# Performance work log

Hardware: AMD Instinct MI355X
Metric: run time of the kernel (lower is better)

Reference implementation:

```python
import jax, jax.numpy as jnp
import numpy as np

N_NODES = 100000
N_EDGES = 1600000
IN, HID, OUT = 512, 128, 64


def setup_inputs() -> dict:
    key = jax.random.key(0)
    ks = jax.random.split(key, 7)
    x = jax.random.normal(ks[0], (N_NODES, IN), dtype=jnp.float32)
    rows = jax.random.randint(ks[1], (N_EDGES,), 0, N_NODES, dtype=jnp.int32)
    cols = jax.random.randint(ks[2], (N_EDGES,), 0, N_NODES, dtype=jnp.int32)
    vals = jax.random.uniform(ks[3], (N_EDGES,), dtype=jnp.float32)
    # torch.nn.Linear weights have shape (out_features, in_features)
    W0 = jax.random.normal(ks[4], (HID, IN), dtype=jnp.float32) * (IN ** -0.5)
    W1 = jax.random.normal(ks[5], (HID, HID), dtype=jnp.float32) * (HID ** -0.5)
    W2 = jax.random.normal(ks[6], (OUT, HID), dtype=jnp.float32) * (HID ** -0.5)
    return {"x": x, "rows": rows, "cols": cols, "vals": vals,
            "W0": W0, "W1": W1, "W2": W2}


def reference(x, rows, cols, vals, W0, W1, W2):
    n = x.shape[0]

    def spmm(h):  # out[r] = sum_e vals[e] * h[cols[e]] for rows[e] == r
        return jax.ops.segment_sum(vals[:, None] * h[cols], rows, num_segments=n)

    # layer 0: Linear -> SpMM -> ReLU (dropout p=0.0 is identity)
    h = jax.nn.relu(spmm(x @ W0.T))
    # layer 1
    h = jax.nn.relu(spmm(h @ W1.T))
    # output layer: Linear -> SpMM (no activation)
    return spmm(h @ W2.T)
```

## Files before the change

kernel.cpp:

```cpp
#include <hip/hip_runtime.h>
#include <hip/hip_bf16.h>
#include <cstddef>


typedef unsigned short ushort_t;
using frag_t = __attribute__((ext_vector_type(8))) short;
using accf4 = __attribute__((ext_vector_type(4))) float;

__device__ __forceinline__ ushort_t f2bf(float f) {
    unsigned int u = __float_as_uint(f);
    u += 0x7FFF + ((u >> 16) & 1);
    return (ushort_t)(u >> 16);
}
__device__ __forceinline__ float bf2f(unsigned int u16) {
    return __uint_as_float(u16 << 16);
}


__global__ __launch_bounds__(256) void init_k(int* __restrict__ cnt8, int m8,
                                              const float* __restrict__ W0,
                                              const float* __restrict__ W1,
                                              const float* __restrict__ W2,
                                              ushort_t* __restrict__ Wb0,
                                              ushort_t* __restrict__ Wb1,
                                              ushort_t* __restrict__ Wb2) {
    int i = blockIdx.x * 256 + threadIdx.x;
    if (i < m8) cnt8[i] = 0;
    if (i < 65536) Wb0[i] = f2bf(W0[i]);
    else if (i < 81920) Wb1[i - 65536] = f2bf(W1[i - 65536]);
    else if (i < 90112) Wb2[i - 81920] = f2bf(W2[i - 81920]);
}


__global__ __launch_bounds__(256) void block_totals(const int* __restrict__ counts,
                                                    int* __restrict__ bsums, int n) {
    __shared__ int s[256];
    int t = threadIdx.x;
    int i = blockIdx.x * 256 + t;
    s[t] = (i < n) ? counts[i] : 0;
    __syncthreads();
    for (int off = 128; off > 0; off >>= 1) {
        if (t < off) s[t] += s[t + off];
        __syncthreads();
    }
    if (t == 0) bsums[blockIdx.x] = s[0];
}

__global__ __launch_bounds__(512) void scan_sums(int* bsums, int nb) {
    __shared__ int s[512];
    int t = threadIdx.x;
    int v = (t < nb) ? bsums[t] : 0;
    s[t] = v;
    __syncthreads();
    for (int off = 1; off < 512; off *= 2) {
        int u = (t >= off) ? s[t - off] : 0;
        __syncthreads();
        s[t] += u;
        __syncthreads();
    }
    if (t < nb) bsums[t] = s[t] - v;
}

__global__ __launch_bounds__(256) void scan_wo(const int* __restrict__ data,
                                               const int* __restrict__ offs,
                                               int* __restrict__ out0, int m) {
    __shared__ int s[256];
    int t = threadIdx.x;
    int i = blockIdx.x * 256 + t;
    int v = (i < m) ? data[i] : 0;
    s[t] = v;
    __syncthreads();
    for (int off = 1; off < 256; off *= 2) {
        int u = (t >= off) ? s[t - off] : 0;
        __syncthreads();
        s[t] += u;
        __syncthreads();
    }
    if (i < m) out0[i] = s[t] - v + offs[blockIdx.x];
}

__global__ __launch_bounds__(256) void scan_final(const int* __restrict__ cnt8,
                                                  const int* __restrict__ offs,
                                                  int* __restrict__ dstbase,
                                                  int* __restrict__ row_ptr,
                                                  int n, int ne, int m8) {
    __shared__ int s[256];
    int t = threadIdx.x;
    int i = blockIdx.x * 256 + t;
    int v = (i < m8) ? cnt8[(i & 7) * n + (i >> 3)] : 0;
    s[t] = v;
    __syncthreads();
    for (int off = 1; off < 256; off *= 2) {
        int u = (t >= off) ? s[t - off] : 0;
        __syncthreads();
        s[t] += u;
        __syncthreads();
    }
    int excl = s[t] - v + offs[blockIdx.x];
    if (i < m8) {
        dstbase[i] = excl;
        if ((i & 7) == 0) row_ptr[i >> 3] = excl;
    }
    if (i == 0) row_ptr[n] = ne;
}


__global__ __launch_bounds__(256) void hist8_k(const int* __restrict__ rows,
                                               int* __restrict__ cnt8,
                                               int* __restrict__ rank,
                                               int n, int ne) {
    int e = blockIdx.x * 256 + threadIdx.x;
    if (e >= ne) return;
    int s = blockIdx.x & 7;
    rank[e] = atomicAdd(&cnt8[s * n + rows[e]], 1);
}

__global__ __launch_bounds__(256) void scatter8_k(const int* __restrict__ rows,
                                                  const int* __restrict__ cols,
                                                  const float* __restrict__ vals,
                                                  const int* __restrict__ dstbase,
                                                  const int* __restrict__ rank,
                                                  int2* __restrict__ es, int ne) {
    int e = blockIdx.x * 256 + threadIdx.x;
    if (e >= ne) return;
    int s = blockIdx.x & 7;
    int r = rows[e];
    int p = dstbase[r * 8 + s] + rank[e];
    es[p] = make_int2(cols[e], __float_as_int(vals[e]));
}


template <int K, int N, int BM, int BN, int BK, bool ABF16>
__global__ __launch_bounds__(256) void gemm_bf16(const void* __restrict__ Av,
                                                 const ushort_t* __restrict__ Wb,
                                                 ushort_t* __restrict__ C, int M) {
    constexpr int WM = BM / 2, WN = BN / 2;
    constexpr int TI = WM / 16, TJ = WN / 16;
    constexpr int LDA = BK + 8;
    constexpr int T = K / BK;
    constexpr int A_PER_F = BM * BK / 4 / 256;
    constexpr int A_PER_B = BM * BK / 8 / 256;
    constexpr int B_PER = BN * BK / 8 / 256;

    __shared__ __align__(16) ushort_t As[BM][LDA];
    __shared__ __align__(16) ushort_t Bs[BN][LDA];

    const int tid = threadIdx.x;
    const int lane = tid & 63;
    const int wid = tid >> 6;
    const int wm = wid >> 1, wn = wid & 1;
    const int rowBase = blockIdx.x * BM;
    const int lrow = lane & 15, kq = lane >> 4;

    float4 aF[ABF16 ? 1 : A_PER_F];
    uint4 aB[ABF16 ? A_PER_B : 1];
    uint4 bR[B_PER];

    auto loadTile = [&](int k0) {
        if constexpr (ABF16) {
            const ushort_t* A = (const ushort_t*)Av;
#pragma unroll
            for (int i = 0; i < A_PER_B; i++) {
                int idx = tid + i * 256;
                int r = idx / (BK / 8), c8 = idx % (BK / 8);
                int grow = rowBase + r;
                aB[i] = (grow < M) ? *(const uint4*)(A + (size_t)grow * K + k0 + c8 * 8)
                                   : make_uint4(0, 0, 0, 0);
            }
        } else {
            const float* A = (const float*)Av;
#pragma unroll
            for (int i = 0; i < A_PER_F; i++) {
                int idx = tid + i * 256;
                int r = idx / (BK / 4), c4 = idx % (BK / 4);
                int grow = rowBase + r;
                aF[i] = (grow < M) ? *(const float4*)(A + (size_t)grow * K + k0 + c4 * 4)
                                   : make_float4(0.f, 0.f, 0.f, 0.f);
            }
        }
#pragma unroll
        for (int i = 0; i < B_PER; i++) {
            int idx = tid + i * 256;
            int r = idx / (BK / 8), c8 = idx % (BK / 8);
            bR[i] = *(const uint4*)(Wb + (size_t)r * K + k0 + c8 * 8);
        }
    };
    auto storeTile = [&]() {
        if constexpr (ABF16) {
#pragma unroll
            for (int i = 0; i < A_PER_B; i++) {
                int idx = tid + i * 256;
                int r = idx / (BK / 8), c8 = idx % (BK / 8);
                *(uint4*)&As[r][c8 * 8] = aB[i];
            }
        } else {
#pragma unroll
            for (int i = 0; i < A_PER_F; i++) {
                int idx = tid + i * 256;
                int r = idx / (BK / 4), c4 = idx % (BK / 4);
                ushort_t p[4] = {f2bf(aF[i].x), f2bf(aF[i].y), f2bf(aF[i].z), f2bf(aF[i].w)};
                *(uint2*)&As[r][c4 * 4] = *(uint2*)p;
            }
        }
#pragma unroll
        for (int i = 0; i < B_PER; i++) {
            int idx = tid + i * 256;
            int r = idx / (BK / 8), c8 = idx % (BK / 8);
            *(uint4*)&Bs[r][c8 * 8] = bR[i];
        }
    };

    accf4 acc[TI][TJ];
#pragma unroll
    for (int i = 0; i < TI; i++)
#pragma unroll
        for (int j = 0; j < TJ; j++) acc[i][j] = accf4{0.f, 0.f, 0.f, 0.f};

    loadTile(0);
    storeTile();
    __syncthreads();

    for (int t = 0; t < T; t++) {
        if (t + 1 < T) loadTile((t + 1) * BK);
#pragma unroll
        for (int ks = 0; ks < BK / 32; ks++) {
            const int kb = ks * 32 + kq * 8;
            frag_t a[TI], b[TJ];
#pragma unroll
            for (int i = 0; i < TI; i++)
                a[i] = *(const frag_t*)&As[wm * WM + i * 16 + lrow][kb];
#pragma unroll
            for (int j = 0; j < TJ; j++)
                b[j] = *(const frag_t*)&Bs[wn * WN + j * 16 + lrow][kb];
#pragma unroll
            for (int i = 0; i < TI; i++)
#pragma unroll
                for (int j = 0; j < TJ; j++)
                    acc[i][j] = __builtin_amdgcn_mfma_f32_16x16x32_bf16(
                        a[i], b[j], acc[i][j], 0, 0, 0);
        }
        __syncthreads();
        if (t + 1 < T) {
            storeTile();
            __syncthreads();
        }
    }

#pragma unroll
    for (int i = 0; i < TI; i++) {
#pragma unroll
        for (int j = 0; j < TJ; j++) {
            int col = wn * WN + j * 16 + lrow;
#pragma unroll
            for (int r = 0; r < 4; r++) {
                int grow = rowBase + wm * WM + i * 16 + kq * 4 + r;
                if (grow < M) C[(size_t)grow * N + col] = f2bf(acc[i][j][r]);
            }
        }
    }
}


__device__ __forceinline__ void acc8(float* acc, uint4 q, float v) {
    acc[0] += v * bf2f(q.x & 0xffff); acc[1] += v * bf2f(q.x >> 16);
    acc[2] += v * bf2f(q.y & 0xffff); acc[3] += v * bf2f(q.y >> 16);
    acc[4] += v * bf2f(q.z & 0xffff); acc[5] += v * bf2f(q.z >> 16);
    acc[6] += v * bf2f(q.w & 0xffff); acc[7] += v * bf2f(q.w >> 16);
}
__device__ __forceinline__ void acc4f(float* acc, uint2 q, float v) {
    acc[0] += v * bf2f(q.x & 0xffff); acc[1] += v * bf2f(q.x >> 16);
    acc[2] += v * bf2f(q.y & 0xffff); acc[3] += v * bf2f(q.y >> 16);
}

template <bool RELU>
__global__ __launch_bounds__(256) void spmm_csr_128(const int* __restrict__ row_ptr,
                                                    const int2* __restrict__ es,
                                                    const ushort_t* __restrict__ G,
                                                    ushort_t* __restrict__ H, int n) {
    int row = blockIdx.x * 4 + (threadIdx.x >> 6);
    int lane = threadIdx.x & 63;
    int g = lane >> 4, lg = lane & 15;
    if (row >= n) return;
    int s = row_ptr[row];
    int e = row_ptr[row + 1];
    float acc[8];
#pragma unroll
    for (int k = 0; k < 8; k++) acc[k] = 0.f;
    const ushort_t* __restrict__ Gp = G + lg * 8;
    int p = s;
    for (; p + 15 < e; p += 16) {
        int2 e0 = es[p + g], e1 = es[p + 4 + g];
        int2 e2 = es[p + 8 + g], e3 = es[p + 12 + g];
        uint4 q0 = *(const uint4*)(Gp + (size_t)e0.x * 128);
        uint4 q1 = *(const uint4*)(Gp + (size_t)e1.x * 128);
        uint4 q2 = *(const uint4*)(Gp + (size_t)e2.x * 128);
        uint4 q3 = *(const uint4*)(Gp + (size_t)e3.x * 128);
        acc8(acc, q0, __int_as_float(e0.y));
        acc8(acc, q1, __int_as_float(e1.y));
        acc8(acc, q2, __int_as_float(e2.y));
        acc8(acc, q3, __int_as_float(e3.y));
    }
    for (; p < e; p += 4) {
        if (p + g < e) {
            int2 e0 = es[p + g];
            uint4 q0 = *(const uint4*)(Gp + (size_t)e0.x * 128);
            acc8(acc, q0, __int_as_float(e0.y));
        }
    }
#pragma unroll
    for (int k = 0; k < 8; k++) {
        acc[k] += __shfl_xor(acc[k], 16);
        acc[k] += __shfl_xor(acc[k], 32);
    }
    if (g == 0) {
        if (RELU) {
#pragma unroll
            for (int k = 0; k < 8; k++) acc[k] = fmaxf(acc[k], 0.f);
        }
        uint4 o;
        o.x = (unsigned)f2bf(acc[0]) | ((unsigned)f2bf(acc[1]) << 16);
        o.y = (unsigned)f2bf(acc[2]) | ((unsigned)f2bf(acc[3]) << 16);
        o.z = (unsigned)f2bf(acc[4]) | ((unsigned)f2bf(acc[5]) << 16);
        o.w = (unsigned)f2bf(acc[6]) | ((unsigned)f2bf(acc[7]) << 16);
        *(uint4*)(H + (size_t)row * 128 + lg * 8) = o;
    }
}

__global__ __launch_bounds__(256) void spmm_csr_64f(const int* __restrict__ row_ptr,
                                                    const int2* __restrict__ es,
                                                    const ushort_t* __restrict__ G,
                                                    float* __restrict__ H, int n) {
    int row = blockIdx.x * 4 + (threadIdx.x >> 6);
    int lane = threadIdx.x & 63;
    int g = lane >> 4, lg = lane & 15;
    if (row >= n) return;
    int s = row_ptr[row];
    int e = row_ptr[row + 1];
    float acc[4] = {0.f, 0.f, 0.f, 0.f};
    const ushort_t* __restrict__ Gp = G + lg * 4;
    int p = s;
    for (; p + 15 < e; p += 16) {
        int2 e0 = es[p + g], e1 = es[p + 4 + g];
        int2 e2 = es[p + 8 + g], e3 = es[p + 12 + g];
        uint2 q0 = *(const uint2*)(Gp + (size_t)e0.x * 64);
        uint2 q1 = *(const uint2*)(Gp + (size_t)e1.x * 64);
        uint2 q2 = *(const uint2*)(Gp + (size_t)e2.x * 64);
        uint2 q3 = *(const uint2*)(Gp + (size_t)e3.x * 64);
        acc4f(acc, q0, __int_as_float(e0.y));
        acc4f(acc, q1, __int_as_float(e1.y));
        acc4f(acc, q2, __int_as_float(e2.y));
        acc4f(acc, q3, __int_as_float(e3.y));
    }
    for (; p < e; p += 4) {
        if (p + g < e) {
            int2 e0 = es[p + g];
            uint2 q0 = *(const uint2*)(Gp + (size_t)e0.x * 64);
            acc4f(acc, q0, __int_as_float(e0.y));
        }
    }
#pragma unroll
    for (int k = 0; k < 4; k++) {
        acc[k] += __shfl_xor(acc[k], 16);
        acc[k] += __shfl_xor(acc[k], 32);
    }
    if (g == 0) {
        float4 o = make_float4(acc[0], acc[1], acc[2], acc[3]);
        *(float4*)(H + (size_t)row * 64 + lg * 4) = o;
    }
}

static inline size_t align_up(size_t x, size_t a) { return (x + a - 1) & ~(a - 1); }

extern "C" void kernel_launch(void* const* d_in, const int* in_sizes, int n_in,
                              void* d_out, int out_size, void* d_ws, size_t ws_size,
                              hipStream_t stream) {
    const float* x = (const float*)d_in[0];
    const int* rows = (const int*)d_in[1];
    const int* cols = (const int*)d_in[2];
    const float* vals = (const float*)d_in[3];
    const float* W0 = (const float*)d_in[4];
    const float* W1 = (const float*)d_in[5];
    const float* W2 = (const float*)d_in[6];
    float* out = (float*)d_out;

    const int IN = 512, HID = 128, OUT = 64;
    const int n = in_sizes[0] / IN;
    const int ne = in_sizes[1];
    (void)OUT;

    char* ws = (char*)d_ws;
    size_t off = 0;
    ushort_t* g = (ushort_t*)(ws + off); off = align_up(off + (size_t)n * HID * 2, 512);
    ushort_t* h = (ushort_t*)(ws + off); off = align_up(off + (size_t)n * HID * 2, 512);
    int2* es2 = (int2*)(ws + off); off = align_up(off + (size_t)ne * 8, 512);
    int* cnt8 = (int*)(ws + off); off = align_up(off + (size_t)8 * n * 4, 512);
    int* rank = (int*)(ws + off); off = align_up(off + (size_t)ne * 4, 512);
    int* dstbase = (int*)(ws + off); off = align_up(off + (size_t)8 * n * 4, 512);
    int* row_ptr = (int*)(ws + off); off = align_up(off + (size_t)(n + 1) * 4, 512);
    int* bsum0 = (int*)(ws + off); off = align_up(off + 4096 * 4, 512);
    int* bsum1 = (int*)(ws + off); off = align_up(off + 512 * 4, 512);
    int* off0 = (int*)(ws + off); off = align_up(off + 4096 * 4, 512);
    ushort_t* Wb0 = (ushort_t*)(ws + off); off = align_up(off + (size_t)HID * IN * 2, 512);
    ushort_t* Wb1 = (ushort_t*)(ws + off); off = align_up(off + (size_t)HID * HID * 2, 512);
    ushort_t* Wb2 = (ushort_t*)(ws + off); off = align_up(off + (size_t)OUT * HID * 2, 512);

    const int eb = (ne + 255) / 256;
    const int m8 = 8 * n;
    const int nb8 = (m8 + 255) / 256;
    const int nb8b = (nb8 + 255) / 256;

    init_k<<<nb8, 256, 0, stream>>>(cnt8, m8, W0, W1, W2, Wb0, Wb1, Wb2);
    hist8_k<<<eb, 256, 0, stream>>>(rows, cnt8, rank, n, ne);
    block_totals<<<nb8, 256, 0, stream>>>(cnt8, bsum0, m8);
    (void)0;
    {
        struct Launcher {};
    }
    extern __global__ void block_totals_t(const int*, int*, int, int);
    block_totals_t<<<nb8, 256, 0, stream>>>(cnt8, bsum0, n, m8);
    block_totals<<<nb8b, 256, 0, stream>>>(bsum0, bsum1, nb8);
    scan_sums<<<1, 512, 0, stream>>>(bsum1, nb8b);
    scan_wo<<<nb8b, 256, 0, stream>>>(bsum0, bsum1, off0, nb8);
    scan_final<<<nb8, 256, 0, stream>>>(cnt8, off0, dstbase, row_ptr, n, ne, m8);
    scatter8_k<<<eb, 256, 0, stream>>>(rows, cols, vals, dstbase, rank, es2, ne);

    const int gblocks = (n + 127) / 128;
    const int sblocks = (n + 3) / 4;

    gemm_bf16<512, 128, 128, 128, 64, false><<<gblocks, 256, 0, stream>>>(x, Wb0, g, n);
    spmm_csr_128<true><<<sblocks, 256, 0, stream>>>(row_ptr, es2, g, h, n);

    gemm_bf16<128, 128, 128, 128, 64, true><<<gblocks, 256, 0, stream>>>(h, Wb1, g, n);
    spmm_csr_128<true><<<sblocks, 256, 0, stream>>>(row_ptr, es2, g, h, n);

    gemm_bf16<128, 64, 128, 64, 64, true><<<gblocks, 256, 0, stream>>>(h, Wb2, g, n);
    spmm_csr_64f<<<sblocks, 256, 0, stream>>>(row_ptr, es2, g, out, n);
}

__global__ __launch_bounds__(256) void block_totals_t(const int* __restrict__ cnt8,
                                                      int* __restrict__ bsums,
                                                      int n, int m8) {
    __shared__ int s[256];
    int t = threadIdx.x;
    int i = blockIdx.x * 256 + t;
    s[t] = (i < m8) ? cnt8[(i & 7) * n + (i >> 3)] : 0;
    __syncthreads();
    for (int off = 128; off > 0; off >>= 1) {
        if (t < off) s[t] += s[t + off];
        __syncthreads();
    }
    if (t == 0) bsums[blockIdx.x] = s[0];
}
```

Before: 661.6 us.

## Fuse layer GEMMs into SpMM epilogues and merge first GEMM with init

Moves the layer-1 and layer-2 dense GEMMs into the epilogue of the preceding SpMM: each block aggregates 16 rows, applies ReLU, stages them in shared memory, and multiplies by the bf16 weights with MFMA before writing. The first GEMM now reads fp32 W0 directly and runs in the same launch as the counter reset and weight conversion. This removes two GEMM launches and their intermediate round trips through global memory, at the cost of fewer threads per row during the gather and extra shared-memory and sync overhead in the SpMM kernels. It also drops a redundant block_totals launch.

Result: no change. 666.7 us (+0.8%).

```diff
diff --git a/kernel.cpp b/kernel.cpp
--- a/kernel.cpp
+++ b/kernel.cpp
@@ -17,18 +17,129 @@
 }
 
 
-__global__ __launch_bounds__(256) void init_k(int* __restrict__ cnt8, int m8,
-                                              const float* __restrict__ W0,
-                                              const float* __restrict__ W1,
-                                              const float* __restrict__ W2,
-                                              ushort_t* __restrict__ Wb0,
-                                              ushort_t* __restrict__ Wb1,
-                                              ushort_t* __restrict__ Wb2) {
-    int i = blockIdx.x * 256 + threadIdx.x;
-    if (i < m8) cnt8[i] = 0;
-    if (i < 65536) Wb0[i] = f2bf(W0[i]);
-    else if (i < 81920) Wb1[i - 65536] = f2bf(W1[i - 65536]);
-    else if (i < 90112) Wb2[i - 81920] = f2bf(W2[i - 81920]);
+__device__ void gemm0_body(int bx, const float* __restrict__ A,
+                           const float* __restrict__ W, ushort_t* __restrict__ C,
+                           int M) {
+    constexpr int K = 512, N = 128, BM = 128, BN = 128, BK = 64;
+    constexpr int WM = BM / 2, WN = BN / 2;
+    constexpr int TI = WM / 16, TJ = WN / 16;
+    constexpr int LDA = BK + 8;
+    constexpr int T = K / BK;
+    constexpr int A_PER = BM * BK / 4 / 256;
+    constexpr int B_PER = BN * BK / 4 / 256;
+
+    __shared__ __align__(16) ushort_t As[BM][LDA];
+    __shared__ __align__(16) ushort_t Bs[BN][LDA];
+
+    const int tid = threadIdx.x;
+    const int lane = tid & 63;
+    const int wid = tid >> 6;
+    const int wm = wid >> 1, wn = wid & 1;
+    const int rowBase = bx * BM;
+    const int lrow = lane & 15, kq = lane >> 4;
+
+    float4 aF[A_PER], bF[B_PER];
+
+    auto loadTile = [&](int k0) {
+#pragma unroll
+        for (int i = 0; i < A_PER; i++) {
+            int idx = tid + i * 256;
+            int r = idx / (BK / 4), c4 = idx % (BK / 4);
+            int grow = rowBase + r;
+            aF[i] = (grow < M) ? *(const float4*)(A + (size_t)grow * K + k0 + c4 * 4)
+                               : make_float4(0.f, 0.f, 0.f, 0.f);
+        }
+#pragma unroll
+        for (int i = 0; i < B_PER; i++) {
+            int idx = tid + i * 256;
+            int r = idx / (BK / 4), c4 = idx % (BK / 4);
+            bF[i] = *(const float4*)(W + (size_t)r * K + k0 + c4 * 4);
+        }
+    };
+    auto storeTile = [&]() {
+#pragma unroll
+        for (int i = 0; i < A_PER; i++) {
+            int idx = tid + i * 256;
+            int r = idx / (BK / 4), c4 = idx % (BK / 4);
+            ushort_t p[4] = {f2bf(aF[i].x), f2bf(aF[i].y), f2bf(aF[i].z), f2bf(aF[i].w)};
+            *(uint2*)&As[r][c4 * 4] = *(uint2*)p;
+        }
+#pragma unroll
+        for (int i = 0; i < B_PER; i++) {
+            int idx = tid + i * 256;
+            int r = idx / (BK / 4), c4 = idx % (BK / 4);
+            ushort_t p[4] = {f2bf(bF[i].x), f2bf(bF[i].y), f2bf(bF[i].z), f2bf(bF[i].w)};
+            *(uint2*)&Bs[r][c4 * 4] = *(uint2*)p;
+        }
+    };
+
+    accf4 acc[TI][TJ];
+#pragma unroll
+    for (int i = 0; i < TI; i++)
+#pragma unroll
+        for (int j = 0; j < TJ; j++) acc[i][j] = accf4{0.f, 0.f, 0.f, 0.f};
+
+    loadTile(0);
+    storeTile();
+    __syncthreads();
+
+    for (int t = 0; t < T; t++) {
+        if (t + 1 < T) loadTile((t + 1) * BK);
+#pragma unroll
+        for (int ks = 0; ks < BK / 32; ks++) {
+            const int kb = ks * 32 + kq * 8;
+            frag_t a[TI], b[TJ];
+#pragma unroll
+            for (int i = 0; i < TI; i++)
+                a[i] = *(const frag_t*)&As[wm * WM + i * 16 + lrow][kb];
+#pragma unroll
+            for (int j = 0; j < TJ; j++)
+                b[j] = *(const frag_t*)&Bs[wn * WN + j * 16 + lrow][kb];
+#pragma unroll
+            for (int i = 0; i < TI; i++)
+#pragma unroll
+                for (int j = 0; j < TJ; j++)
+                    acc[i][j] = __builtin_amdgcn_mfma_f32_16x16x32_bf16(
+                        a[i], b[j], acc[i][j], 0, 0, 0);
+        }
+        __syncthreads();
+        if (t + 1 < T) {
+            storeTile();
+            __syncthreads();
+        }
+    }
+
+#pragma unroll
+    for (int i = 0; i < TI; i++) {
+#pragma unroll
+        for (int j = 0; j < TJ; j++) {
+            int col = wn * WN + j * 16 + lrow;
+#pragma unroll
+            for (int r = 0; r < 4; r++) {
+                int grow = rowBase + wm * WM + i * 16 + kq * 4 + r;
+                if (grow < M) C[(size_t)grow * N + col] = f2bf(acc[i][j][r]);
+            }
+        }
+    }
+}
+
+__global__ __launch_bounds__(256) void d1_k(const float* __restrict__ x,
+                                            const float* __restrict__ W0,
+                                            ushort_t* __restrict__ g0, int M,
+                                            int* __restrict__ cnt8, int m8,
+                                            const float* __restrict__ W1,
+                                            const float* __restrict__ W2,
+                                            ushort_t* __restrict__ Wb1,
+                                            ushort_t* __restrict__ Wb2,
+                                            int gblocks) {
+    if ((int)blockIdx.x < gblocks) {
+        gemm0_body(blockIdx.x, x, W0, g0, M);
+    } else {
+        int i = ((int)blockIdx.x - gblocks) * 256 + threadIdx.x;
+        if (i < m8) cnt8[i] = 0;
+        if (i < 16384) Wb1[i] = f2bf(W1[i]);
+        else if (i < 24576) Wb2[i - 16384] = f2bf(W2[i - 16384]);
+    }
 }
 
 
@@ -38,6 +149,21 @@
     int t = threadIdx.x;
     int i = blockIdx.x * 256 + t;
     s[t] = (i < n) ? counts[i] : 0;
+    __syncthreads();
+    for (int off = 128; off > 0; off >>= 1) {
+        if (t < off) s[t] += s[t + off];
+        __syncthreads();
+    }
+    if (t == 0) bsums[blockIdx.x] = s[0];
+}
+
+__global__ __launch_bounds__(256) void block_totals_t(const int* __restrict__ cnt8,
+                                                      int* __restrict__ bsums,
+                                                      int n, int m8) {
+    __shared__ int s[256];
+    int t = threadIdx.x;
+    int i = blockIdx.x * 256 + t;
+    s[t] = (i < m8) ? cnt8[(i & 7) * n + (i >> 3)] : 0;
     __syncthreads();
     for (int off = 128; off > 0; off >>= 1) {
         if (t < off) s[t] += s[t + off];
@@ -130,137 +256,6 @@
 }
 
 
-template <int K, int N, int BM, int BN, int BK, bool ABF16>
-__global__ __launch_bounds__(256) void gemm_bf16(const void* __restrict__ Av,
-                                                 const ushort_t* __restrict__ Wb,
-                                                 ushort_t* __restrict__ C, int M) {
-    constexpr int WM = BM / 2, WN = BN / 2;
-    constexpr int TI = WM / 16, TJ = WN / 16;
-    constexpr int LDA = BK + 8;
-    constexpr int T = K / BK;
-    constexpr int A_PER_F = BM * BK / 4 / 256;
-    constexpr int A_PER_B = BM * BK / 8 / 256;
-    constexpr int B_PER = BN * BK / 8 / 256;
-
-    __shared__ __align__(16) ushort_t As[BM][LDA];
-    __shared__ __align__(16) ushort_t Bs[BN][LDA];
-
-    const int tid = threadIdx.x;
-    const int lane = tid & 63;
-    const int wid = tid >> 6;
-    const int wm = wid >> 1, wn = wid & 1;
-    const int rowBase = blockIdx.x * BM;
-    const int lrow = lane & 15, kq = lane >> 4;
-
-    float4 aF[ABF16 ? 1 : A_PER_F];
-    uint4 aB[ABF16 ? A_PER_B : 1];
-    uint4 bR[B_PER];
-
-    auto loadTile = [&](int k0) {
-        if constexpr (ABF16) {
-            const ushort_t* A = (const ushort_t*)Av;
-#pragma unroll
-            for (int i = 0; i < A_PER_B; i++) {
-                int idx = tid + i * 256;
-                int r = idx / (BK / 8), c8 = idx % (BK / 8);
-                int grow = rowBase + r;
-                aB[i] = (grow < M) ? *(const uint4*)(A + (size_t)grow * K + k0 + c8 * 8)
-                                   : make_uint4(0, 0, 0, 0);
-            }
-        } else {
-            const float* A = (const float*)Av;
-#pragma unroll
-            for (int i = 0; i < A_PER_F; i++) {
-                int idx = tid + i * 256;
-                int r = idx / (BK / 4), c4 = idx % (BK / 4);
-                int grow = rowBase + r;
-                aF[i] = (grow < M) ? *(const float4*)(A + (size_t)grow * K + k0 + c4 * 4)
-                                   : make_float4(0.f, 0.f, 0.f, 0.f);
-            }
-        }
-#pragma unroll
-        for (int i = 0; i < B_PER; i++) {
-            int idx = tid + i * 256;
-            int r = idx / (BK / 8), c8 = idx % (BK / 8);
-            bR[i] = *(const uint4*)(Wb + (size_t)r * K + k0 + c8 * 8);
-        }
-    };
-    auto storeTile = [&]() {
-        if constexpr (ABF16) {
-#pragma unroll
-            for (int i = 0; i < A_PER_B; i++) {
-                int idx = tid + i * 256;
-                int r = idx / (BK / 8), c8 = idx % (BK / 8);
-                *(uint4*)&As[r][c8 * 8] = aB[i];
-            }
-        } else {
-#pragma unroll
-            for (int i = 0; i < A_PER_F; i++) {
-                int idx = tid + i * 256;
-                int r = idx / (BK / 4), c4 = idx % (BK / 4);
-                ushort_t p[4] = {f2bf(aF[i].x), f2bf(aF[i].y), f2bf(aF[i].z), f2bf(aF[i].w)};
-                *(uint2*)&As[r][c4 * 4] = *(uint2*)p;
-            }
-        }
-#pragma unroll
-        for (int i = 0; i < B_PER; i++) {
-            int idx = tid + i * 256;
-            int r = idx / (BK / 8), c8 = idx % (BK / 8);
-            *(uint4*)&Bs[r][c8 * 8] = bR[i];
-        }
-    };
-
-    accf4 acc[TI][TJ];
-#pragma unroll
-    for (int i = 0; i < TI; i++)
-#pragma unroll
-        for (int j = 0; j < TJ; j++) acc[i][j] = accf4{0.f, 0.f, 0.f, 0.f};
-
-    loadTile(0);
-    storeTile();
-    __syncthreads();
-
-    for (int t = 0; t < T; t++) {
-        if (t + 1 < T) loadTile((t + 1) * BK);
-#pragma unroll
-        for (int ks = 0; ks < BK / 32; ks++) {
-            const int kb = ks * 32 + kq * 8;
-            frag_t a[TI], b[TJ];
-#pragma unroll
-            for (int i = 0; i < TI; i++)
-                a[i] = *(const frag_t*)&As[wm * WM + i * 16 + lrow][kb];
-#pragma unroll
-            for (int j = 0; j < TJ; j++)
-                b[j] = *(const frag_t*)&Bs[wn * WN + j * 16 + lrow][kb];
-#pragma unroll
-            for (int i = 0; i < TI; i++)
-#pragma unroll
-                for (int j = 0; j < TJ; j++)
-                    acc[i][j] = __builtin_amdgcn_mfma_f32_16x16x32_bf16(
-                        a[i], b[j], acc[i][j], 0, 0, 0);
-        }
-        __syncthreads();
-        if (t + 1 < T) {
-            storeTile();
-            __syncthreads();
-        }
-    }
-
-#pragma unroll
-    for (int i = 0; i < TI; i++) {
-#pragma unroll
-        for (int j = 0; j < TJ; j++) {
-            int col = wn * WN + j * 16 + lrow;
-#pragma unroll
-            for (int r = 0; r < 4; r++) {
-                int grow = rowBase + wm * WM + i * 16 + kq * 4 + r;
-                if (grow < M) C[(size_t)grow * N + col] = f2bf(acc[i][j][r]);
-            }
-        }
-    }
-}
-
-
 __device__ __forceinline__ void acc8(float* acc, uint4 q, float v) {
     acc[0] += v * bf2f(q.x & 0xffff); acc[1] += v * bf2f(q.x >> 16);
     acc[2] += v * bf2f(q.y & 0xffff); acc[3] += v * bf2f(q.y >> 16);
@@ -272,59 +267,101 @@
     acc[2] += v * bf2f(q.y & 0xffff); acc[3] += v * bf2f(q.y >> 16);
 }
 
-template <bool RELU>
-__global__ __launch_bounds__(256) void spmm_csr_128(const int* __restrict__ row_ptr,
-                                                    const int2* __restrict__ es,
-                                                    const ushort_t* __restrict__ G,
-                                                    ushort_t* __restrict__ H, int n) {
-    int row = blockIdx.x * 4 + (threadIdx.x >> 6);
-    int lane = threadIdx.x & 63;
-    int g = lane >> 4, lg = lane & 15;
-    if (row >= n) return;
-    int s = row_ptr[row];
-    int e = row_ptr[row + 1];
-    float acc[8];
-#pragma unroll
-    for (int k = 0; k < 8; k++) acc[k] = 0.f;
+template <int NOUT>
+__global__ __launch_bounds__(256) void spmm_mfma(const int* __restrict__ row_ptr,
+                                                 const int2* __restrict__ es,
+                                                 const ushort_t* __restrict__ G,
+                                                 const ushort_t* __restrict__ Wb,
+                                                 ushort_t* __restrict__ Hout, int n) {
+    constexpr int TJ = NOUT / 64;
+    constexpr int SEG = NOUT / 8;
+
+    __shared__ __align__(16) ushort_t Hs[16][136];
+    __shared__ __align__(16) ushort_t Os[16][NOUT + 8];
+
+    const int tid = threadIdx.x;
+    const int lane = tid & 63;
+    const int wid = tid >> 6;
+    const int g = lane >> 4, lg = lane & 15;
+    const int lrow = lane & 15, kq = lane >> 4;
+    const int rowBase = blockIdx.x * 16;
+
+    frag_t bfr[4][TJ];
+#pragma unroll
+    for (int ks = 0; ks < 4; ks++)
+#pragma unroll
+        for (int j = 0; j < TJ; j++)
+            bfr[ks][j] = *(const frag_t*)&Wb[(size_t)(wid * 16 * TJ + j * 16 + lrow) * 128 +
+                                             ks * 32 + kq * 8];
+
     const ushort_t* __restrict__ Gp = G + lg * 8;
-    int p = s;
-    for (; p + 15 < e; p += 16) {
-        int2 e0 = es[p + g], e1 = es[p + 4 + g];
-        int2 e2 = es[p + 8 + g], e3 = es[p + 12 + g];
-        uint4 q0 = *(const uint4*)(Gp + (size_t)e0.x * 128);
-        uint4 q1 = *(const uint4*)(Gp + (size_t)e1.x * 128);
-        uint4 q2 = *(const uint4*)(Gp + (size_t)e2.x * 128);
-        uint4 q3 = *(const uint4*)(Gp + (size_t)e3.x * 128);
-        acc8(acc, q0, __int_as_float(e0.y));
-        acc8(acc, q1, __int_as_float(e1.y));
-        acc8(acc, q2, __int_as_float(e2.y));
-        acc8(acc, q3, __int_as_float(e3.y));
-    }
-    for (; p < e; p += 4) {
-        if (p + g < e) {
-            int2 e0 = es[p + g];
-            uint4 q0 = *(const uint4*)(Gp + (size_t)e0.x * 128);
-            acc8(acc, q0, __int_as_float(e0.y));
-        }
-    }
-#pragma unroll
-    for (int k = 0; k < 8; k++) {
-        acc[k] += __shfl_xor(acc[k], 16);
-        acc[k] += __shfl_xor(acc[k], 32);
-    }
-    if (g == 0) {
-        if (RELU) {
-#pragma unroll
-            for (int k = 0; k < 8; k++) acc[k] = fmaxf(acc[k], 0.f);
-        }
-        uint4 o;
-        o.x = (unsigned)f2bf(acc[0]) | ((unsigned)f2bf(acc[1]) << 16);
-        o.y = (unsigned)f2bf(acc[2]) | ((unsigned)f2bf(acc[3]) << 16);
-        o.z = (unsigned)f2bf(acc[4]) | ((unsigned)f2bf(acc[5]) << 16);
-        o.w = (unsigned)f2bf(acc[6]) | ((unsigned)f2bf(acc[7]) << 16);
-        *(uint4*)(H + (size_t)row * 128 + lg * 8) = o;
-    }
-}
+#pragma unroll
+    for (int q = 0; q < 4; q++) {
+        int row = rowBase + wid * 4 + q;
+        float acc[8];
+#pragma unroll
+        for (int k = 0; k < 8; k++) acc[k] = 0.f;
+        if (row < n) {
+            int s = row_ptr[row];
+            int e = row_ptr[row + 1];
+            for (int p = s; p < e; p += 16) {
+#pragma unroll
+                for (int u = 0; u < 4; u++) {
+                    int idx = p + u * 4 + g;
+                    if (idx < e) {
+                        int2 ed = es[idx];
+                        uint4 qv = *(const uint4*)(Gp + (size_t)ed.x * 128);
+                        acc8(acc, qv, __int_as_float(ed.y));
+                    }
+                }
+            }
+        }
+#pragma unroll
+        for (int k = 0; k < 8; k++) {
+            acc[k] += __shfl_xor(acc[k], 16);
+            acc[k] += __shfl_xor(acc[k], 32);
+        }
+        if (g == 0) {
+            uint4 o;
+            float a0 = fmaxf(acc[0], 0.f), a1 = fmaxf(acc[1], 0.f);
+            float a2 = fmaxf(acc[2], 0.f), a3 = fmaxf(acc[3], 0.f);
+            float a4 = fmaxf(acc[4], 0.f), a5 = fmaxf(acc[5], 0.f);
+            float a6 = fmaxf(acc[6], 0.f), a7 = fmaxf(acc[7], 0.f);
+            o.x = (unsigned)f2bf(a0) | ((unsigned)f2bf(a1) << 16);
+            o.y = (unsigned)f2bf(a2) | ((unsigned)f2bf(a3) << 16);
+            o.z = (unsigned)f2bf(a4) | ((unsigned)f2bf(a5) << 16);
+            o.w = (unsigned)f2bf(a6) | ((unsigned)f2bf(a7) << 16);
+            *(uint4*)&Hs[wid * 4 + q][lg * 8] = o;
+        }
+    }
+    __syncthreads();
+
+    accf4 oacc[TJ];
+#pragma unroll
+    for (int j = 0; j < TJ; j++) oacc[j] = accf4{0.f, 0.f, 0.f, 0.f};
+#pragma unroll
+    for (int ks = 0; ks < 4; ks++) {
+        frag_t a = *(const frag_t*)&Hs[lrow][ks * 32 + kq * 8];
+#pragma unroll
+        for (int j = 0; j < TJ; j++)
+            oacc[j] = __builtin_amdgcn_mfma_f32_16x16x32_bf16(a, bfr[ks][j], oacc[j], 0, 0, 0);
+    }
+#pragma unroll
+    for (int j = 0; j < TJ; j++) {
+        int col = wid * 16 * TJ + j * 16 + lrow;
+#pragma unroll
+        for (int r = 0; r < 4; r++) Os[kq * 4 + r][col] = f2bf(oacc[j][r]);
+    }
+    __syncthreads();
+
+    if (tid < 16 * SEG) {
+        int row16 = tid / SEG, sg = tid % SEG;
+        if (rowBase + row16 < n)
+            *(uint4*)&Hout[(size_t)(rowBase + row16) * NOUT + sg * 8] =
+                *(const uint4*)&Os[row16][sg * 8];
+    }
+}
+
 
 __global__ __launch_bounds__(256) void spmm_csr_64f(const int* __restrict__ row_ptr,
                                                     const int2* __restrict__ es,
@@ -338,24 +375,15 @@
     int e = row_ptr[row + 1];
     float acc[4] = {0.f, 0.f, 0.f, 0.f};
     const ushort_t* __restrict__ Gp = G + lg * 4;
-    int p = s;
-    for (; p + 15 < e; p += 16) {
-        int2 e0 = es[p + g], e1 = es[p + 4 + g];
-        int2 e2 = es[p + 8 + g], e3 = es[p + 12 + g];
-        uint2 q0 = *(const uint2*)(Gp + (size_t)e0.x * 64);
-        uint2 q1 = *(const uint2*)(Gp + (size_t)e1.x * 64);
-        uint2 q2 = *(const uint2*)(Gp + (size_t)e2.x * 64);
-        uint2 q3 = *(const uint2*)(Gp + (size_t)e3.x * 64);
-        acc4f(acc, q0, __int_as_float(e0.y));
-        acc4f(acc, q1, __int_as_float(e1.y));
-        acc4f(acc, q2, __int_as_float(e2.y));
-        acc4f(acc, q3, __int_as_float(e3.y));
-    }
-    for (; p < e; p += 4) {
-        if (p + g < e) {
-            int2 e0 = es[p + g];
-            uint2 q0 = *(const uint2*)(Gp + (size_t)e0.x * 64);
-            acc4f(acc, q0, __int_as_float(e0.y));
+    for (int p = s; p < e; p += 16) {
+#pragma unroll
+        for (int u = 0; u < 4; u++) {
+            int idx = p + u * 4 + g;
+            if (idx < e) {
+                int2 e0 = es[idx];
+                uint2 q0 = *(const uint2*)(Gp + (size_t)e0.x * 64);
+                acc4f(acc, q0, __int_as_float(e0.y));
+            }
         }
     }
 #pragma unroll
@@ -390,8 +418,9 @@
 
     char* ws = (char*)d_ws;
     size_t off = 0;
-    ushort_t* g = (ushort_t*)(ws + off); off = align_up(off + (size_t)n * HID * 2, 512);
-    ushort_t* h = (ushort_t*)(ws + off); off = align_up(off + (size_t)n * HID * 2, 512);
+    ushort_t* g0 = (ushort_t*)(ws + off); off = align_up(off + (size_t)n * HID * 2, 512);
+    ushort_t* g1 = (ushort_t*)(ws + off); off = align_up(off + (size_t)n * HID * 2, 512);
+    ushort_t* g2 = (ushort_t*)(ws + off); off = align_up(off + (size_t)n * 64 * 2, 512);
     int2* es2 = (int2*)(ws + off); off = align_up(off + (size_t)ne * 8, 512);
     int* cnt8 = (int*)(ws + off); off = align_up(off + (size_t)8 * n * 4, 512);
     int* rank = (int*)(ws + off); off = align_up(off + (size_t)ne * 4, 512);
@@ -400,23 +429,21 @@
     int* bsum0 = (int*)(ws + off); off = align_up(off + 4096 * 4, 512);
     int* bsum1 = (int*)(ws + off); off = align_up(off + 512 * 4, 512);
     int* off0 = (int*)(ws + off); off = align_up(off + 4096 * 4, 512);
-    ushort_t* Wb0 = (ushort_t*)(ws + off); off = align_up(off + (size_t)HID * IN * 2, 512);
     ushort_t* Wb1 = (ushort_t*)(ws + off); off = align_up(off + (size_t)HID * HID * 2, 512);
-    ushort_t* Wb2 = (ushort_t*)(ws + off); off = align_up(off + (size_t)OUT * HID * 2, 512);
+    ushort_t* Wb2 = (ushort_t*)(ws + off); off = align_up(off + (size_t)64 * HID * 2, 512);
 
     const int eb = (ne + 255) / 256;
     const int m8 = 8 * n;
     const int nb8 = (m8 + 255) / 256;
     const int nb8b = (nb8 + 255) / 256;
-
-    init_k<<<nb8, 256, 0, stream>>>(cnt8, m8, W0, W1, W2, Wb0, Wb1, Wb2);
+    const int gblocks = (n + 127) / 128;
+    const int fblocks = (n + 15) / 16;
+    const int sblocks = (n + 3) / 4;
+
+    d1_k<<<gblocks + nb8, 256, 0, stream>>>(x, W0, g0, n, cnt8, m8, W1, W2,
+                                            Wb1, Wb2, gblocks);
+
     hist8_k<<<eb, 256, 0, stream>>>(rows, cnt8, rank, n, ne);
-    block_totals<<<nb8, 256, 0, stream>>>(cnt8, bsum0, m8);
-    (void)0;
-    {
-        struct Launcher {};
-    }
-    extern __global__ void block_totals_t(const int*, int*, int, int);
     block_totals_t<<<nb8, 256, 0, stream>>>(cnt8, bsum0, n, m8);
     block_totals<<<nb8b, 256, 0, stream>>>(bsum0, bsum1, nb8);
     scan_sums<<<1, 512, 0, stream>>>(bsum1, nb8b);
@@ -424,30 +451,7 @@
     scan_final<<<nb8, 256, 0, stream>>>(cnt8, off0, dstbase, row_ptr, n, ne, m8);
     scatter8_k<<<eb, 256, 0, stream>>>(rows, cols, vals, dstbase, rank, es2, ne);
 
-    const int gblocks = (n + 127) / 128;
-    const int sblocks = (n + 3) / 4;
-
-    gemm_bf16<512, 128, 128, 128, 64, false><<<gblocks, 256, 0, stream>>>(x, Wb0, g, n);
-    spmm_csr_128<true><<<sblocks, 256, 0, stream>>>(row_ptr, es2, g, h, n);
-
-    gemm_bf16<128, 128, 128, 128, 64, true><<<gblocks, 256, 0, stream>>>(h, Wb1, g, n);
-    spmm_csr_128<true><<<sblocks, 256, 0, stream>>>(row_ptr, es2, g, h, n);
-
-    gemm_bf16<128, 64, 128, 64, 64, true><<<gblocks, 256, 0, stream>>>(h, Wb2, g, n);
-    spmm_csr_64f<<<sblocks, 256, 0, stream>>>(row_ptr, es2, g, out, n);
-}
-
-__global__ __launch_bounds__(256) void block_totals_t(const int* __restrict__ cnt8,
-                                                      int* __restrict__ bsums,
-                                                      int n, int m8) {
-    __shared__ int s[256];
-    int t = threadIdx.x;
-    int i = blockIdx.x * 256 + t;
-    s[t] = (i < m8) ? cnt8[(i & 7) * n + (i >> 3)] : 0;
-    __syncthreads();
-    for (int off = 128; off > 0; off >>= 1) {
-        if (t < off) s[t] += s[t + off];
-        __syncthreads();
-    }
-    if (t == 0) bsums[blockIdx.x] = s[0];
-}
+    spmm_mfma<128><<<fblocks, 256, 0, stream>>>(row_ptr, es2, g0, Wb1, g1, n);
+    spmm_mfma<64><<<fblocks, 256, 0, stream>>>(row_ptr, es2, g1, Wb2, g2, n);
+    spmm_csr_64f<<<sblocks, 256, 0, stream>>>(row_ptr, es2, g2, out, n);
+}
```
